# Performance work log

Measured on AMD Instinct MI355X. Metric: run time of the kernel, lower is better.

## Reference

```python
import jax, jax.numpy as jnp
import numpy as np

HEAD_SIZE = 64
D_MODEL = 1024


def setup_inputs() -> dict:
    key = jax.random.key(0)
    ks = jax.random.split(key, 6)
    B, S, D, H = 4, 4096, D_MODEL, HEAD_SIZE
    q = jax.random.normal(ks[0], (B, S, D), dtype=jnp.float32)
    k = jax.random.normal(ks[1], (B, S, D), dtype=jnp.float32)
    v = jax.random.normal(ks[2], (B, S, D), dtype=jnp.float32)
    # Linear(d_model, head_size, bias=False): stored as [D, H] so x @ W
    scale = 1.0 / np.sqrt(D)
    w_q = jax.random.normal(ks[3], (D, H), dtype=jnp.float32) * scale
    w_k = jax.random.normal(ks[4], (D, H), dtype=jnp.float32) * scale
    w_v = jax.random.normal(ks[5], (D, H), dtype=jnp.float32) * scale
    return {"q": q, "k": k, "v": v, "w_q": w_q, "w_k": w_k, "w_v": w_v}


def reference(q, k, v, w_q, w_k, w_v):
    # project: [B,S,D] @ [D,H] -> [B,S,H]
    qh = q @ w_q
    kh = k @ w_k
    vh = v @ w_v
    H = qh.shape[-1]
    # scores [B,S,S], scaled by head_size**-0.5
    rel = jnp.einsum('bqh,bkh->bqk', qh, kh) * (H ** -0.5)
    S = rel.shape[-1]
    causal = jnp.tril(jnp.ones((S, S), dtype=bool))
    rel = jnp.where(causal, rel, -jnp.inf)
    weights = jax.nn.softmax(rel, axis=-1)
    return jnp.einsum('bqk,bkh->bqh', weights, vh)
```

## Files before the change

kernel.cpp:

```cpp
#include <hip/hip_runtime.h>
#include <hip/hip_bf16.h>
#include <cstdint>

#define D_MODEL 1024
#define HEAD    64
#define SEQ     4096
#define BATCH   4
#define NROWS   (BATCH * SEQ)

typedef __attribute__((ext_vector_type(8))) short short8;
typedef __attribute__((ext_vector_type(4))) float floatx4;

__device__ __forceinline__ ushort f2bf(float f) {
    union { __hip_bfloat16 h; ushort u; } c;
    c.h = __float2bfloat16(f);
    return c.u;
}
__device__ __forceinline__ uint pk2(float a, float b) {
    return (uint)f2bf(a) | ((uint)f2bf(b) << 16);
}

__global__ __launch_bounds__(256) void wprep_kernel(
    const float* __restrict__ wq, const float* __restrict__ wk,
    const float* __restrict__ wv, ushort* __restrict__ wt)
{
    const int which = blockIdx.y;
    const int k0    = blockIdx.x * 64;
    const float* w  = (which == 0) ? wq : (which == 1) ? wk : wv;
    const int tid   = threadIdx.x;

    __shared__ ushort lds[64][65];

#pragma unroll
    for (int i = 0; i < 16; ++i) {
        int idx = tid + 256 * i;
        int kl  = idx >> 6;
        int n   = idx & 63;
        lds[n][kl] = f2bf(w[(size_t)(k0 + kl) * 64 + n]);
    }
    __syncthreads();
#pragma unroll
    for (int i = 0; i < 16; ++i) {
        int idx = tid + 256 * i;
        int n   = idx >> 6;
        int kl  = idx & 63;
        wt[(size_t)(which * 64 + n) * D_MODEL + k0 + kl] = lds[n][kl];
    }
}

__global__ __launch_bounds__(64) void proj_kernel(
    const float* __restrict__ xq, const float* __restrict__ xk,
    const float* __restrict__ xv, const ushort* __restrict__ wt,
    ushort* __restrict__ qh, ushort* __restrict__ kh, ushort* __restrict__ vt)
{
    const int which = blockIdx.y;
    const float*  x = (which == 0) ? xq : (which == 1) ? xk : xv;
    const ushort* w = wt + (size_t)which * 64 * D_MODEL;

    const int row0 = blockIdx.x * 16;
    const int l16  = threadIdx.x & 15;
    const int quad = threadIdx.x >> 4;

    const float* xr = x + (size_t)(row0 + l16) * D_MODEL + quad * 8;
    const ushort* wr[4];
#pragma unroll
    for (int nt = 0; nt < 4; ++nt)
        wr[nt] = w + (size_t)(nt * 16 + l16) * D_MODEL + quad * 8;

    floatx4 acc[4] = {};

    float4 xc[4];
    short8 wc[8];
    xc[0] = *(const float4*)(xr + 0);  xc[1] = *(const float4*)(xr + 4);
    xc[2] = *(const float4*)(xr + 32); xc[3] = *(const float4*)(xr + 36);
#pragma unroll
    for (int nt = 0; nt < 4; ++nt) {
        wc[nt * 2]     = *(const short8*)(wr[nt]);
        wc[nt * 2 + 1] = *(const short8*)(wr[nt] + 32);
    }

    for (int kk = 0; kk < D_MODEL; kk += 64) {
        const int nk = (kk + 64 < D_MODEL) ? kk + 64 : kk;
        float4 xn[4];
        short8 wn[8];
        xn[0] = *(const float4*)(xr + nk + 0);  xn[1] = *(const float4*)(xr + nk + 4);
        xn[2] = *(const float4*)(xr + nk + 32); xn[3] = *(const float4*)(xr + nk + 36);
#pragma unroll
        for (int nt = 0; nt < 4; ++nt) {
            wn[nt * 2]     = *(const short8*)(wr[nt] + nk);
            wn[nt * 2 + 1] = *(const short8*)(wr[nt] + nk + 32);
        }

        union { short8 s; uint u[4]; } a0, a1;
        a0.u[0] = pk2(xc[0].x, xc[0].y); a0.u[1] = pk2(xc[0].z, xc[0].w);
        a0.u[2] = pk2(xc[1].x, xc[1].y); a0.u[3] = pk2(xc[1].z, xc[1].w);
        a1.u[0] = pk2(xc[2].x, xc[2].y); a1.u[1] = pk2(xc[2].z, xc[2].w);
        a1.u[2] = pk2(xc[3].x, xc[3].y); a1.u[3] = pk2(xc[3].z, xc[3].w);

#pragma unroll
        for (int nt = 0; nt < 4; ++nt) {
            acc[nt] = __builtin_amdgcn_mfma_f32_16x16x32_bf16(a0.s, wc[nt * 2],     acc[nt], 0, 0, 0);
            acc[nt] = __builtin_amdgcn_mfma_f32_16x16x32_bf16(a1.s, wc[nt * 2 + 1], acc[nt], 0, 0, 0);
        }
#pragma unroll
        for (int i = 0; i < 4; ++i) xc[i] = xn[i];
#pragma unroll
        for (int i = 0; i < 8; ++i) wc[i] = wn[i];
    }

    if (which < 2) {
        ushort* y = (which == 0) ? qh : kh;
        const float sc = (which == 0) ? 0.125f : 1.0f;
#pragma unroll
        for (int nt = 0; nt < 4; ++nt) {
            int h = nt * 16 + l16;
#pragma unroll
            for (int r = 0; r < 4; ++r)
                y[(size_t)(row0 + quad * 4 + r) * HEAD + h] = f2bf(acc[nt][r] * sc);
        }
    } else {
        int gm0 = row0 + quad * 4;
        int b   = gm0 >> 12;
        int s0  = gm0 & (SEQ - 1);
#pragma unroll
        for (int nt = 0; nt < 4; ++nt) {
            int h = nt * 16 + l16;
            uint2 pk = make_uint2(pk2(acc[nt][0], acc[nt][1]), pk2(acc[nt][2], acc[nt][3]));
            *(uint2*)&vt[(size_t)(b * 64 + h) * SEQ + s0] = pk;
        }
    }
}

__global__ __launch_bounds__(256, 2) void attn_kernel(
    const ushort* __restrict__ qh, const ushort* __restrict__ kh,
    const ushort* __restrict__ vt, float* __restrict__ out)
{
    const int b    = blockIdx.x >> 7;
    const int i    = blockIdx.x & 127;
    const int qsA  = i, qsB = 255 - i;
    const int q0A  = qsA * 16, q0B = qsB * 16;
    const int nA   = (qsA >> 2) + 1;
    const int nB   = (qsB >> 2) + 1;
    const int tid  = threadIdx.x;
    const int wv   = tid >> 6;
    const int ln   = tid & 63;
    const int l16  = ln & 15;
    const int quad = ln >> 4;

    __shared__ ushort PA[4][16 * 72];
    __shared__ ushort PB[4][16 * 72];
    __shared__ float  Obuf[4][16][68];
    __shared__ float  Lbuf[4][16];

    const ushort* khb = kh + (size_t)b * SEQ * HEAD;
    const ushort* vtb = vt + (size_t)b * HEAD * SEQ;

    const size_t qbA = ((size_t)b * SEQ + q0A + l16) * HEAD + quad * 8;
    const size_t qbB = ((size_t)b * SEQ + q0B + l16) * HEAD + quad * 8;
    const short8 qA0 = *(const short8*)(qh + qbA);
    const short8 qA1 = *(const short8*)(qh + qbA + 32);
    const short8 qB0 = *(const short8*)(qh + qbB);
    const short8 qB1 = *(const short8*)(qh + qbB + 32);

    floatx4 OA[4] = {}, OB[4] = {};
    float rsA = 0.f, rsB = 0.f;
    ushort* myPA = PA[wv];
    ushort* myPB = PB[wv];

    const int cA = (nA > wv) ? (((nA - 1 - wv) >> 2) + 1) : 0;
    const int cB = ((nB - 1 - wv) >> 2) + 1;
    const int steps = (cA > cB) ? cA : cB;

    for (int s = 0; s < steps; ++s) {
        const int ktA = wv + 4 * s, ktB = wv + 4 * s;
        const bool doA = s < cA, doB = s < cB;
        const int k0A = ktA * 64, k0B = ktB * 64;

        short8 kfA[8], vfA[8], kfB[8], vfB[8];
        if (doA) {
#pragma unroll
            for (int nt = 0; nt < 4; ++nt) {
                const ushort* vp = vtb + (size_t)(nt * 16 + l16) * SEQ + k0A + quad * 8;
                vfA[nt * 2] = *(const short8*)vp; vfA[nt * 2 + 1] = *(const short8*)(vp + 32);
                const ushort* kp = khb + (size_t)(k0A + nt * 16 + l16) * HEAD + quad * 8;
                kfA[nt * 2] = *(const short8*)kp; kfA[nt * 2 + 1] = *(const short8*)(kp + 32);
            }
        }
        if (doB) {
#pragma unroll
            for (int nt = 0; nt < 4; ++nt) {
                const ushort* vp = vtb + (size_t)(nt * 16 + l16) * SEQ + k0B + quad * 8;
                vfB[nt * 2] = *(const short8*)vp; vfB[nt * 2 + 1] = *(const short8*)(vp + 32);
                const ushort* kp = khb + (size_t)(k0B + nt * 16 + l16) * HEAD + quad * 8;
                kfB[nt * 2] = *(const short8*)kp; kfB[nt * 2 + 1] = *(const short8*)(kp + 32);
            }
        }

        floatx4 aA[4], aB[4];
        if (doA) {
#pragma unroll
            for (int nt = 0; nt < 4; ++nt) {
                floatx4 c = {};
                c = __builtin_amdgcn_mfma_f32_16x16x32_bf16(kfA[nt * 2],     qA0, c, 0, 0, 0);
                c = __builtin_amdgcn_mfma_f32_16x16x32_bf16(kfA[nt * 2 + 1], qA1, c, 0, 0, 0);
                aA[nt] = c;
            }
        }
        if (doB) {
#pragma unroll
            for (int nt = 0; nt < 4; ++nt) {
                floatx4 c = {};
                c = __builtin_amdgcn_mfma_f32_16x16x32_bf16(kfB[nt * 2],     qB0, c, 0, 0, 0);
                c = __builtin_amdgcn_mfma_f32_16x16x32_bf16(kfB[nt * 2 + 1], qB1, c, 0, 0, 0);
                aB[nt] = c;
            }
        }

        if (doA) {
            const bool masked = (ktA == nA - 1);
#pragma unroll
            for (int nt = 0; nt < 4; ++nt) {
                union { ushort u[4]; uint2 w; } pk;
#pragma unroll
                for (int r = 0; r < 4; ++r) {
                    float sv = aA[nt][r];
                    if (masked && (k0A + nt * 16 + quad * 4 + r > q0A + l16)) sv = -3.0e38f;
                    float p = __expf(sv);
                    rsA += p;
                    pk.u[r] = f2bf(p);
                }
                *(uint2*)&myPA[l16 * 72 + nt * 16 + quad * 4] = pk.w;
            }
        }
        if (doB) {
            const bool masked = (ktB == nB - 1);
#pragma unroll
            for (int nt = 0; nt < 4; ++nt) {
                union { ushort u[4]; uint2 w; } pk;
#pragma unroll
                for (int r = 0; r < 4; ++r) {
                    float sv = aB[nt][r];
                    if (masked && (k0B + nt * 16 + quad * 4 + r > q0B + l16)) sv = -3.0e38f;
                    float p = __expf(sv);
                    rsB += p;
                    pk.u[r] = f2bf(p);
                }
                *(uint2*)&myPB[l16 * 72 + nt * 16 + quad * 4] = pk.w;
            }
        }

        if (doA) {
            short8 p0 = *(const short8*)&myPA[l16 * 72 + quad * 8];
            short8 p1 = *(const short8*)&myPA[l16 * 72 + 32 + quad * 8];
#pragma unroll
            for (int nt = 0; nt < 4; ++nt) {
                OA[nt] = __builtin_amdgcn_mfma_f32_16x16x32_bf16(p0, vfA[nt * 2],     OA[nt], 0, 0, 0);
                OA[nt] = __builtin_amdgcn_mfma_f32_16x16x32_bf16(p1, vfA[nt * 2 + 1], OA[nt], 0, 0, 0);
            }
        }
        if (doB) {
            short8 p0 = *(const short8*)&myPB[l16 * 72 + quad * 8];
            short8 p1 = *(const short8*)&myPB[l16 * 72 + 32 + quad * 8];
#pragma unroll
            for (int nt = 0; nt < 4; ++nt) {
                OB[nt] = __builtin_amdgcn_mfma_f32_16x16x32_bf16(p0, vfB[nt * 2],     OB[nt], 0, 0, 0);
                OB[nt] = __builtin_amdgcn_mfma_f32_16x16x32_bf16(p1, vfB[nt * 2 + 1], OB[nt], 0, 0, 0);
            }
        }
    }

    rsA += __shfl_xor(rsA, 16); rsA += __shfl_xor(rsA, 32);
    if (quad == 0) Lbuf[wv][l16] = rsA;
#pragma unroll
    for (int nt = 0; nt < 4; ++nt)
#pragma unroll
        for (int r = 0; r < 4; ++r)
            Obuf[wv][quad * 4 + r][nt * 16 + l16] = OA[nt][r];
    __syncthreads();
    {
        const int row = tid >> 4, h0 = (tid & 15) * 4;
        float l = Lbuf[0][row] + Lbuf[1][row] + Lbuf[2][row] + Lbuf[3][row];
        float inv = 1.f / l;
        float4 o;
        o.x = (Obuf[0][row][h0+0] + Obuf[1][row][h0+0] + Obuf[2][row][h0+0] + Obuf[3][row][h0+0]) * inv;
        o.y = (Obuf[0][row][h0+1] + Obuf[1][row][h0+1] + Obuf[2][row][h0+1] + Obuf[3][row][h0+1]) * inv;
        o.z = (Obuf[0][row][h0+2] + Obuf[1][row][h0+2] + Obuf[2][row][h0+2] + Obuf[3][row][h0+2]) * inv;
        o.w = (Obuf[0][row][h0+3] + Obuf[1][row][h0+3] + Obuf[2][row][h0+3] + Obuf[3][row][h0+3]) * inv;
        *(float4*)&out[((size_t)b * SEQ + q0A + row) * HEAD + h0] = o;
    }
    __syncthreads();

    rsB += __shfl_xor(rsB, 16); rsB += __shfl_xor(rsB, 32);
    if (quad == 0) Lbuf[wv][l16] = rsB;
#pragma unroll
    for (int nt = 0; nt < 4; ++nt)
#pragma unroll
        for (int r = 0; r < 4; ++r)
            Obuf[wv][quad * 4 + r][nt * 16 + l16] = OB[nt][r];
    __syncthreads();
    {
        const int row = tid >> 4, h0 = (tid & 15) * 4;
        float l = Lbuf[0][row] + Lbuf[1][row] + Lbuf[2][row] + Lbuf[3][row];
        float inv = 1.f / l;
        float4 o;
        o.x = (Obuf[0][row][h0+0] + Obuf[1][row][h0+0] + Obuf[2][row][h0+0] + Obuf[3][row][h0+0]) * inv;
        o.y = (Obuf[0][row][h0+1] + Obuf[1][row][h0+1] + Obuf[2][row][h0+1] + Obuf[3][row][h0+1]) * inv;
        o.z = (Obuf[0][row][h0+2] + Obuf[1][row][h0+2] + Obuf[2][row][h0+2] + Obuf[3][row][h0+2]) * inv;
        o.w = (Obuf[0][row][h0+3] + Obuf[1][row][h0+3] + Obuf[2][row][h0+3] + Obuf[3][row][h0+3]) * inv;
        *(float4*)&out[((size_t)b * SEQ + q0B + row) * HEAD + h0] = o;
    }
}

extern "C" void kernel_launch(void* const* d_in, const int* in_sizes, int n_in,
                              void* d_out, int out_size, void* d_ws, size_t ws_size,
                              hipStream_t stream) {
    const float* q  = (const float*)d_in[0];
    const float* k  = (const float*)d_in[1];
    const float* v  = (const float*)d_in[2];
    const float* wq = (const float*)d_in[3];
    const float* wk = (const float*)d_in[4];
    const float* wv = (const float*)d_in[5];

    ushort* qh = (ushort*)d_ws;
    ushort* kh = qh + (size_t)NROWS * HEAD;
    ushort* vt = kh + (size_t)NROWS * HEAD;
    ushort* wt = vt + (size_t)NROWS * HEAD;

    dim3 wgrid(D_MODEL / 64, 3);
    wprep_kernel<<<wgrid, 256, 0, stream>>>(wq, wk, wv, wt);

    dim3 pgrid(NROWS / 16, 3);
    proj_kernel<<<pgrid, 64, 0, stream>>>(q, k, v, wt, qh, kh, vt);

    attn_kernel<<<BATCH * 128, 256, 0, stream>>>(qh, kh, vt, (float*)d_out);
}
```

Baseline: 291.4 us.

## Split projection K-dimension across four waves with LDS reduction

The projection kernel goes from one 64-thread wave per 16-row tile to four waves. Each wave covers a quarter of the 1024-wide reduction dimension, and the partial MFMA accumulators are summed through shared memory before the bf16 outputs are written. The aim is a shorter serial loop per wave and more memory-level parallelism for the bandwidth-bound fp32 input reads. The cost is extra LDS traffic, a block barrier, and an extra reduction step.

```diff
diff --git a/kernel.cpp b/kernel.cpp
--- a/kernel.cpp
+++ b/kernel.cpp
@@ -48,7 +48,7 @@
     }
 }
 
-__global__ __launch_bounds__(64) void proj_kernel(
+__global__ __launch_bounds__(256) void proj_kernel(
     const float* __restrict__ xq, const float* __restrict__ xk,
     const float* __restrict__ xv, const ushort* __restrict__ wt,
     ushort* __restrict__ qh, ushort* __restrict__ kh, ushort* __restrict__ vt)
@@ -58,14 +58,17 @@
     const ushort* w = wt + (size_t)which * 64 * D_MODEL;
 
     const int row0 = blockIdx.x * 16;
-    const int l16  = threadIdx.x & 15;
-    const int quad = threadIdx.x >> 4;
-
-    const float* xr = x + (size_t)(row0 + l16) * D_MODEL + quad * 8;
+    const int tid  = threadIdx.x;
+    const int wv   = tid >> 6;
+    const int l16  = tid & 15;
+    const int quad = (tid >> 4) & 3;
+    const int kbase = wv * 256;
+
+    const float* xr = x + (size_t)(row0 + l16) * D_MODEL + kbase + quad * 8;
     const ushort* wr[4];
 #pragma unroll
     for (int nt = 0; nt < 4; ++nt)
-        wr[nt] = w + (size_t)(nt * 16 + l16) * D_MODEL + quad * 8;
+        wr[nt] = w + (size_t)(nt * 16 + l16) * D_MODEL + kbase + quad * 8;
 
     floatx4 acc[4] = {};
 
@@ -79,8 +82,8 @@
         wc[nt * 2 + 1] = *(const short8*)(wr[nt] + 32);
     }
 
-    for (int kk = 0; kk < D_MODEL; kk += 64) {
-        const int nk = (kk + 64 < D_MODEL) ? kk + 64 : kk;
+    for (int kk = 0; kk < 256; kk += 64) {
+        const int nk = (kk + 64 < 256) ? kk + 64 : kk;
         float4 xn[4];
         short8 wn[8];
         xn[0] = *(const float4*)(xr + nk + 0);  xn[1] = *(const float4*)(xr + nk + 4);
@@ -108,26 +111,40 @@
         for (int i = 0; i < 8; ++i) wc[i] = wn[i];
     }
 
+    __shared__ float red[4][16][68];
+#pragma unroll
+    for (int nt = 0; nt < 4; ++nt)
+#pragma unroll
+        for (int r = 0; r < 4; ++r)
+            red[wv][quad * 4 + r][nt * 16 + l16] = acc[nt][r];
+    __syncthreads();
+
     if (which < 2) {
         ushort* y = (which == 0) ? qh : kh;
         const float sc = (which == 0) ? 0.125f : 1.0f;
-#pragma unroll
-        for (int nt = 0; nt < 4; ++nt) {
-            int h = nt * 16 + l16;
-#pragma unroll
-            for (int r = 0; r < 4; ++r)
-                y[(size_t)(row0 + quad * 4 + r) * HEAD + h] = f2bf(acc[nt][r] * sc);
-        }
+        const int row = tid >> 4;
+        const int h0  = (tid & 15) * 4;
+        union { ushort u[4]; uint2 w2; } pk;
+#pragma unroll
+        for (int j = 0; j < 4; ++j) {
+            float s = red[0][row][h0 + j] + red[1][row][h0 + j]
+                    + red[2][row][h0 + j] + red[3][row][h0 + j];
+            pk.u[j] = f2bf(s * sc);
+        }
+        *(uint2*)&y[(size_t)(row0 + row) * HEAD + h0] = pk.w2;
     } else {
-        int gm0 = row0 + quad * 4;
-        int b   = gm0 >> 12;
-        int s0  = gm0 & (SEQ - 1);
-#pragma unroll
-        for (int nt = 0; nt < 4; ++nt) {
-            int h = nt * 16 + l16;
-            uint2 pk = make_uint2(pk2(acc[nt][0], acc[nt][1]), pk2(acc[nt][2], acc[nt][3]));
-            *(uint2*)&vt[(size_t)(b * 64 + h) * SEQ + s0] = pk;
-        }
+        const int h  = tid & 63;
+        const int s0 = (tid >> 6) * 4;
+        const int b  = row0 >> 12;
+        const int sg = (row0 & (SEQ - 1)) + s0;
+        union { ushort u[4]; uint2 w2; } pk;
+#pragma unroll
+        for (int j = 0; j < 4; ++j) {
+            float s = red[0][s0 + j][h] + red[1][s0 + j][h]
+                    + red[2][s0 + j][h] + red[3][s0 + j][h];
+            pk.u[j] = f2bf(s);
+        }
+        *(uint2*)&vt[(size_t)(b * 64 + h) * SEQ + sg] = pk.w2;
     }
 }
 
@@ -330,7 +347,7 @@
     wprep_kernel<<<wgrid, 256, 0, stream>>>(wq, wk, wv, wt);
 
     dim3 pgrid(NROWS / 16, 3);
-    proj_kernel<<<pgrid, 64, 0, stream>>>(q, k, v, wt, qh, kh, vt);
+    proj_kernel<<<pgrid, 256, 0, stream>>>(q, k, v, wt, qh, kh, vt);
 
     attn_kernel<<<BATCH * 128, 256, 0, stream>>>(qh, kh, vt, (float*)d_out);
 }
```

After: 285.1 us. 2.2% less time.

## Stage projection tiles through LDS with async global_load_lds double buffering

Applied to the files above, without the earlier changes.

The projection kernel now uses 256-thread blocks covering 64 rows. Each K-step stages the fp32 activation tile and the bf16 weight tile into XOR-swizzled, double-buffered shared memory using direct global-to-LDS loads. The goal is to share one weight tile across four waves instead of reloading it per 16-row wave, and to overlap the next tile's loads with the current MFMAs. The cost is 48KB of LDS per block, which limits occupancy, plus a barrier on every K-step.

```diff
diff --git a/kernel.cpp b/kernel.cpp
--- a/kernel.cpp
+++ b/kernel.cpp
@@ -18,6 +18,12 @@
 }
 __device__ __forceinline__ uint pk2(float a, float b) {
     return (uint)f2bf(a) | ((uint)f2bf(b) << 16);
+}
+
+__device__ __forceinline__ void gload16(const void* g, void* l) {
+    __builtin_amdgcn_global_load_lds(
+        (const __attribute__((address_space(1))) unsigned int*)g,
+        (__attribute__((address_space(3))) unsigned int*)l, 16, 0, 0);
 }
 
 __global__ __launch_bounds__(256) void wprep_kernel(
@@ -48,7 +54,7 @@
     }
 }
 
-__global__ __launch_bounds__(64) void proj_kernel(
+__global__ __launch_bounds__(256) void proj_kernel(
     const float* __restrict__ xq, const float* __restrict__ xk,
     const float* __restrict__ xv, const ushort* __restrict__ wt,
     ushort* __restrict__ qh, ushort* __restrict__ kh, ushort* __restrict__ vt)
@@ -57,57 +63,83 @@
     const float*  x = (which == 0) ? xq : (which == 1) ? xk : xv;
     const ushort* w = wt + (size_t)which * 64 * D_MODEL;
 
-    const int row0 = blockIdx.x * 16;
-    const int l16  = threadIdx.x & 15;
-    const int quad = threadIdx.x >> 4;
-
-    const float* xr = x + (size_t)(row0 + l16) * D_MODEL + quad * 8;
-    const ushort* wr[4];
-#pragma unroll
-    for (int nt = 0; nt < 4; ++nt)
-        wr[nt] = w + (size_t)(nt * 16 + l16) * D_MODEL + quad * 8;
+    const int row0 = blockIdx.x * 64;
+    const int tid  = threadIdx.x;
+    const int wv   = tid >> 6;
+    const int ln   = tid & 63;
+    const int l16  = ln & 15;
+    const int quad = ln >> 4;
+
+    __shared__ float  Abuf[2][64 * 64];
+    __shared__ ushort Wbuf[2][64 * 64];
+
+    const float* asrc[4];
+#pragma unroll
+    for (int i = 0; i < 4; ++i) {
+        int j  = wv * 4 + i;
+        int lr = 4 * j + (ln >> 4);
+        int cf = ((ln & 15) ^ (lr & 15)) * 4;
+        asrc[i] = x + (size_t)(row0 + lr) * D_MODEL + cf;
+    }
+    const ushort* wsrc[2];
+#pragma unroll
+    for (int i = 0; i < 2; ++i) {
+        int j  = wv * 2 + i;
+        int n  = 8 * j + (ln >> 3);
+        int kc = ((ln & 7) ^ (ln >> 3)) * 8;
+        wsrc[i] = w + (size_t)n * D_MODEL + kc;
+    }
 
     floatx4 acc[4] = {};
 
-    float4 xc[4];
-    short8 wc[8];
-    xc[0] = *(const float4*)(xr + 0);  xc[1] = *(const float4*)(xr + 4);
-    xc[2] = *(const float4*)(xr + 32); xc[3] = *(const float4*)(xr + 36);
-#pragma unroll
-    for (int nt = 0; nt < 4; ++nt) {
-        wc[nt * 2]     = *(const short8*)(wr[nt]);
-        wc[nt * 2 + 1] = *(const short8*)(wr[nt] + 32);
-    }
-
-    for (int kk = 0; kk < D_MODEL; kk += 64) {
-        const int nk = (kk + 64 < D_MODEL) ? kk + 64 : kk;
-        float4 xn[4];
-        short8 wn[8];
-        xn[0] = *(const float4*)(xr + nk + 0);  xn[1] = *(const float4*)(xr + nk + 4);
-        xn[2] = *(const float4*)(xr + nk + 32); xn[3] = *(const float4*)(xr + nk + 36);
-#pragma unroll
-        for (int nt = 0; nt < 4; ++nt) {
-            wn[nt * 2]     = *(const short8*)(wr[nt] + nk);
-            wn[nt * 2 + 1] = *(const short8*)(wr[nt] + nk + 32);
-        }
-
-        union { short8 s; uint u[4]; } a0, a1;
-        a0.u[0] = pk2(xc[0].x, xc[0].y); a0.u[1] = pk2(xc[0].z, xc[0].w);
-        a0.u[2] = pk2(xc[1].x, xc[1].y); a0.u[3] = pk2(xc[1].z, xc[1].w);
-        a1.u[0] = pk2(xc[2].x, xc[2].y); a1.u[1] = pk2(xc[2].z, xc[2].w);
-        a1.u[2] = pk2(xc[3].x, xc[3].y); a1.u[3] = pk2(xc[3].z, xc[3].w);
-
-#pragma unroll
-        for (int nt = 0; nt < 4; ++nt) {
-            acc[nt] = __builtin_amdgcn_mfma_f32_16x16x32_bf16(a0.s, wc[nt * 2],     acc[nt], 0, 0, 0);
-            acc[nt] = __builtin_amdgcn_mfma_f32_16x16x32_bf16(a1.s, wc[nt * 2 + 1], acc[nt], 0, 0, 0);
-        }
-#pragma unroll
-        for (int i = 0; i < 4; ++i) xc[i] = xn[i];
-#pragma unroll
-        for (int i = 0; i < 8; ++i) wc[i] = wn[i];
-    }
-
+#define STAGE(buf, kk)                                                        \
+    do {                                                                      \
+        char* ab_ = (char*)&Abuf[buf][0];                                     \
+        char* wb_ = (char*)&Wbuf[buf][0];                                     \
+        _Pragma("unroll")                                                     \
+        for (int i_ = 0; i_ < 4; ++i_)                                        \
+            gload16(asrc[i_] + (kk), ab_ + (wv * 4 + i_) * 1024);             \
+        _Pragma("unroll")                                                     \
+        for (int i_ = 0; i_ < 2; ++i_)                                        \
+            gload16(wsrc[i_] + (kk), wb_ + (wv * 2 + i_) * 1024);             \
+    } while (0)
+
+#define COMPUTE(buf)                                                          \
+    do {                                                                      \
+        const char* ab_ = (const char*)&Abuf[buf][0];                         \
+        const char* wb_ = (const char*)&Wbuf[buf][0];                         \
+        const int arow_ = wv * 16 + l16;                                      \
+        const int akey_ = l16 << 4;                         \
+        _Pragma("unroll")                                                     \
+        for (int ks_ = 0; ks_ < 2; ++ks_) {                                   \
+            const int colb_ = (ks_ * 32 + quad * 8) * 4;                      \
+            float4 f0 = *(const float4*)(ab_ + arow_ * 256 + ((colb_)      ^ akey_)); \
+            float4 f1 = *(const float4*)(ab_ + arow_ * 256 + ((colb_ + 16) ^ akey_)); \
+            union { short8 s; uint u[4]; } a_;                                \
+            a_.u[0] = pk2(f0.x, f0.y); a_.u[1] = pk2(f0.z, f0.w);             \
+            a_.u[2] = pk2(f1.x, f1.y); a_.u[3] = pk2(f1.z, f1.w);             \
+            const int wcolb_ = (ks_ * 32 + quad * 8) * 2;                     \
+            const int wkey_  = (l16 & 7) << 4;     \
+            _Pragma("unroll")                                                 \
+            for (int nt_ = 0; nt_ < 4; ++nt_) {                               \
+                const int n_ = nt_ * 16 + l16;                                \
+                short8 bf_ = *(const short8*)(wb_ + n_ * 128 + (wcolb_ ^ wkey_)); \
+                acc[nt_] = __builtin_amdgcn_mfma_f32_16x16x32_bf16(a_.s, bf_, acc[nt_], 0, 0, 0); \
+            }                                                                 \
+        }                                                                     \
+    } while (0)
+
+    STAGE(0, 0);
+    __syncthreads();
+    for (int t = 0; t < 16; ++t) {
+        if (t + 1 < 16) STAGE((t + 1) & 1, (t + 1) * 64);
+        COMPUTE(t & 1);
+        __syncthreads();
+    }
+#undef STAGE
+#undef COMPUTE
+
+    const int rbase = row0 + wv * 16 + quad * 4;
     if (which < 2) {
         ushort* y = (which == 0) ? qh : kh;
         const float sc = (which == 0) ? 0.125f : 1.0f;
@@ -116,12 +148,11 @@
             int h = nt * 16 + l16;
 #pragma unroll
             for (int r = 0; r < 4; ++r)
-                y[(size_t)(row0 + quad * 4 + r) * HEAD + h] = f2bf(acc[nt][r] * sc);
+                y[(size_t)(rbase + r) * HEAD + h] = f2bf(acc[nt][r] * sc);
         }
     } else {
-        int gm0 = row0 + quad * 4;
-        int b   = gm0 >> 12;
-        int s0  = gm0 & (SEQ - 1);
+        const int b  = rbase >> 12;
+        const int s0 = rbase & (SEQ - 1);
 #pragma unroll
         for (int nt = 0; nt < 4; ++nt) {
             int h = nt * 16 + l16;
@@ -329,8 +360,8 @@
     dim3 wgrid(D_MODEL / 64, 3);
     wprep_kernel<<<wgrid, 256, 0, stream>>>(wq, wk, wv, wt);
 
-    dim3 pgrid(NROWS / 16, 3);
-    proj_kernel<<<pgrid, 64, 0, stream>>>(q, k, v, wt, qh, kh, vt);
+    dim3 pgrid(NROWS / 64, 3);
+    proj_kernel<<<pgrid, 256, 0, stream>>>(q, k, v, wt, qh, kh, vt);
 
     attn_kernel<<<BATCH * 128, 256, 0, stream>>>(qh, kh, vt, (float*)d_out);
 }
```

After: 268.7 us. 7.8% less time.

## Stage projection activations through LDS with async global_load_lds double buffering

Applied to the files above, without the earlier changes.

The projection kernel now loads x tiles straight into a double-buffered, XOR-swizzled LDS area using global_load_lds, fully coalesced at 128 columns per stage. Manual vmcnt waits overlap the next tile's loads with the MFMAs on the current one. Weight fragments are read from global per stage. This targets the poorly coalesced strided fp32 activation reads in the projection. It relies on hand-tuned waitcnt counts and has no block barrier, which is only safe because the block is a single wavefront.

```diff
diff --git a/kernel.cpp b/kernel.cpp
--- a/kernel.cpp
+++ b/kernel.cpp
@@ -18,6 +18,12 @@
 }
 __device__ __forceinline__ uint pk2(float a, float b) {
     return (uint)f2bf(a) | ((uint)f2bf(b) << 16);
+}
+
+__device__ __forceinline__ void gload16(const void* g, void* l) {
+    __builtin_amdgcn_global_load_lds(
+        (const __attribute__((address_space(1))) unsigned int*)g,
+        (__attribute__((address_space(3))) unsigned int*)l, 16, 0, 0);
 }
 
 __global__ __launch_bounds__(256) void wprep_kernel(
@@ -58,56 +64,67 @@
     const ushort* w = wt + (size_t)which * 64 * D_MODEL;
 
     const int row0 = blockIdx.x * 16;
-    const int l16  = threadIdx.x & 15;
-    const int quad = threadIdx.x >> 4;
-
-    const float* xr = x + (size_t)(row0 + l16) * D_MODEL + quad * 8;
-    const ushort* wr[4];
-#pragma unroll
-    for (int nt = 0; nt < 4; ++nt)
-        wr[nt] = w + (size_t)(nt * 16 + l16) * D_MODEL + quad * 8;
+    const int ln   = threadIdx.x;
+    const int l16  = ln & 15;
+    const int quad = ln >> 4;
+
+    __shared__ alignas(16) char Ab[2][8192];
+
+    const float* aS[8];
+#pragma unroll
+    for (int j = 0; j < 8; ++j) {
+        int r = 2 * j + (ln >> 5);
+        aS[j] = x + (size_t)(row0 + r) * D_MODEL + (((ln & 31) ^ (r & 7)) << 2);
+    }
 
     floatx4 acc[4] = {};
-
-    float4 xc[4];
-    short8 wc[8];
-    xc[0] = *(const float4*)(xr + 0);  xc[1] = *(const float4*)(xr + 4);
-    xc[2] = *(const float4*)(xr + 32); xc[3] = *(const float4*)(xr + 36);
-#pragma unroll
-    for (int nt = 0; nt < 4; ++nt) {
-        wc[nt * 2]     = *(const short8*)(wr[nt]);
-        wc[nt * 2 + 1] = *(const short8*)(wr[nt] + 32);
-    }
-
-    for (int kk = 0; kk < D_MODEL; kk += 64) {
-        const int nk = (kk + 64 < D_MODEL) ? kk + 64 : kk;
-        float4 xn[4];
-        short8 wn[8];
-        xn[0] = *(const float4*)(xr + nk + 0);  xn[1] = *(const float4*)(xr + nk + 4);
-        xn[2] = *(const float4*)(xr + nk + 32); xn[3] = *(const float4*)(xr + nk + 36);
-#pragma unroll
-        for (int nt = 0; nt < 4; ++nt) {
-            wn[nt * 2]     = *(const short8*)(wr[nt] + nk);
-            wn[nt * 2 + 1] = *(const short8*)(wr[nt] + nk + 32);
-        }
-
-        union { short8 s; uint u[4]; } a0, a1;
-        a0.u[0] = pk2(xc[0].x, xc[0].y); a0.u[1] = pk2(xc[0].z, xc[0].w);
-        a0.u[2] = pk2(xc[1].x, xc[1].y); a0.u[3] = pk2(xc[1].z, xc[1].w);
-        a1.u[0] = pk2(xc[2].x, xc[2].y); a1.u[1] = pk2(xc[2].z, xc[2].w);
-        a1.u[2] = pk2(xc[3].x, xc[3].y); a1.u[3] = pk2(xc[3].z, xc[3].w);
-
-#pragma unroll
-        for (int nt = 0; nt < 4; ++nt) {
-            acc[nt] = __builtin_amdgcn_mfma_f32_16x16x32_bf16(a0.s, wc[nt * 2],     acc[nt], 0, 0, 0);
-            acc[nt] = __builtin_amdgcn_mfma_f32_16x16x32_bf16(a1.s, wc[nt * 2 + 1], acc[nt], 0, 0, 0);
-        }
-#pragma unroll
-        for (int i = 0; i < 4; ++i) xc[i] = xn[i];
-#pragma unroll
-        for (int i = 0; i < 8; ++i) wc[i] = wn[i];
-    }
-
+    const int akey = l16 & 7;
+
+    __builtin_amdgcn_sched_barrier(0);
+#pragma unroll
+    for (int j = 0; j < 8; ++j)
+        gload16(aS[j], &Ab[0][j * 1024]);
+    __builtin_amdgcn_sched_barrier(0);
+
+    for (int t = 0; t < 8; ++t) {
+        short8 wf[16];
+#pragma unroll
+        for (int ks = 0; ks < 4; ++ks)
+#pragma unroll
+            for (int nt = 0; nt < 4; ++nt)
+                wf[ks * 4 + nt] = *(const short8*)(
+                    w + (size_t)(nt * 16 + l16) * D_MODEL + t * 128 + ks * 32 + quad * 8);
+
+        if (t < 7) {
+            __builtin_amdgcn_sched_barrier(0);
+#pragma unroll
+            for (int j = 0; j < 8; ++j)
+                gload16(aS[j] + (t + 1) * 128, &Ab[(t + 1) & 1][j * 1024]);
+            __builtin_amdgcn_sched_barrier(0);
+            asm volatile("s_waitcnt vmcnt(24)" ::: "memory");
+        } else {
+            asm volatile("s_waitcnt vmcnt(16)" ::: "memory");
+        }
+        __builtin_amdgcn_sched_barrier(0);
+
+        const char* ab = &Ab[t & 1][0];
+#pragma unroll
+        for (int ks = 0; ks < 4; ++ks) {
+            const int s0 = ks * 8 + quad * 2;
+            const int p0 = ((s0)     ^ akey) << 4;
+            const int p1 = ((s0 + 1) ^ akey) << 4;
+            float4 f0 = *(const float4*)(ab + l16 * 512 + p0);
+            float4 f1 = *(const float4*)(ab + l16 * 512 + p1);
+            union { short8 s; uint u[4]; } a_;
+            a_.u[0] = pk2(f0.x, f0.y); a_.u[1] = pk2(f0.z, f0.w);
+            a_.u[2] = pk2(f1.x, f1.y); a_.u[3] = pk2(f1.z, f1.w);
+#pragma unroll
+            for (int nt = 0; nt < 4; ++nt)
+                acc[nt] = __builtin_amdgcn_mfma_f32_16x16x32_bf16(a_.s, wf[ks * 4 + nt], acc[nt], 0, 0, 0);
+        }
+    }
+
+    const int rbase = row0 + quad * 4;
     if (which < 2) {
         ushort* y = (which == 0) ? qh : kh;
         const float sc = (which == 0) ? 0.125f : 1.0f;
@@ -116,12 +133,11 @@
             int h = nt * 16 + l16;
 #pragma unroll
             for (int r = 0; r < 4; ++r)
-                y[(size_t)(row0 + quad * 4 + r) * HEAD + h] = f2bf(acc[nt][r] * sc);
+                y[(size_t)(rbase + r) * HEAD + h] = f2bf(acc[nt][r] * sc);
         }
     } else {
-        int gm0 = row0 + quad * 4;
-        int b   = gm0 >> 12;
-        int s0  = gm0 & (SEQ - 1);
+        const int b  = rbase >> 12;
+        const int s0 = rbase & (SEQ - 1);
 #pragma unroll
         for (int nt = 0; nt < 4; ++nt) {
             int h = nt * 16 + l16;
```

After: 289.4 us. Within noise of the previous version (-0.7%).
